# Kernel optimization log

Measured on AMD Instinct MI355X. Metric: run time of the kernel, lower is better.

## Reference

```python
import jax, jax.numpy as jnp
import numpy as np

DIM = 1024
NUM_HEADS = 16
HEAD_DIM = DIM // NUM_HEADS
SCALE = HEAD_DIM ** -0.5
NEG = -1e9


def setup_inputs() -> dict:
    key = jax.random.key(0)
    ks = jax.random.split(key, 10)
    B, N, M, C = 8, 1024, 1024, DIM
    q = jax.random.normal(ks[0], (B, N, C), jnp.float32)
    k = jax.random.normal(ks[1], (B, M, C), jnp.float32)
    v = jax.random.normal(ks[2], (B, M, C), jnp.float32)
    mask = jax.random.randint(ks[3], (B, N), 0, 2, jnp.int32)
    target_mask = jax.random.randint(ks[4], (B, N, M), 0, 2, jnp.int32)
    Wq = jax.random.normal(ks[5], (C, C), jnp.float32) * 0.02
    Wk = jax.random.normal(ks[6], (C, C), jnp.float32) * 0.02
    Wv = jax.random.normal(ks[7], (C, C), jnp.float32) * 0.02
    Wo = jax.random.normal(ks[8], (C, C), jnp.float32) * 0.02
    bo = jnp.zeros((C,), jnp.float32)
    return {"q": q, "k": k, "v": v, "mask": mask, "target_mask": target_mask,
            "Wq": Wq, "Wk": Wk, "Wv": Wv, "Wo": Wo, "bo": bo}


def reference(q, k, v, mask, target_mask, Wq, Wk, Wv, Wo, bo):
    B, N, C = q.shape
    M = k.shape[1]
    H, D = NUM_HEADS, HEAD_DIM
    qh = (q @ Wq).reshape(B, N, H, D)
    kh = (k @ Wk).reshape(B, M, H, D)
    vh = (v @ Wv).reshape(B, M, H, D)
    attn = jnp.einsum('bnhd,bmhd->bhnm', qh, kh) * SCALE  # (B,H,N,M)
    # self-attn key mask (B,N) -> broadcast over queries (requires N==M as in original)
    attn = jnp.where(mask[:, None, None, :] == 0, NEG, attn)
    # cross-attn mask (B,N,M) -> broadcast over heads
    attn = jnp.where(target_mask[:, None, :, :] == 0, NEG, attn)
    attn = jax.nn.softmax(attn, axis=-1)
    x = jnp.einsum('bhnm,bmhd->bnhd', attn, vh).reshape(B, N, C)
    return x @ Wo + bo
```

## Files before the change

### kernel.cpp

```cpp
#include <hip/hip_runtime.h>
#include <hip/hip_bf16.h>

#define DEV __device__ __forceinline__

typedef __attribute__((ext_vector_type(8))) short bf16x8;
typedef __attribute__((ext_vector_type(4))) short s16x4;
typedef __attribute__((ext_vector_type(4))) float f32x4;
typedef unsigned int u32;
typedef unsigned long long u64;

DEV short f2bf(float f) {
  union { float f; u32 u; } x; x.f = f;
  u32 r = x.u + 0x7fffu + ((x.u >> 16) & 1u);
  return (short)(r >> 16);
}

DEV void gload_lds16(const void* g, void* l) {
  __builtin_amdgcn_global_load_lds(
      (const __attribute__((address_space(1))) u32*)g,
      (__attribute__((address_space(3))) u32*)l, 16, 0, 0);
}

__global__ __launch_bounds__(256) void pack_mask(const int* __restrict__ mask,
                                                 const int* __restrict__ tmask,
                                                 u64* __restrict__ pk) {
  int bn = blockIdx.x;
  int b = bn >> 10;
  int t = threadIdx.x, w = t >> 6, lane = t & 63;
  const int* tr = tmask + (size_t)bn * 1024;
  const int* mr = mask + b * 1024;
#pragma unroll
  for (int it = 0; it < 4; ++it) {
    int m = it * 256 + w * 64 + lane;
    bool on = (mr[m] != 0) && (tr[m] != 0);
    u64 bits = __ballot(on);
    if (lane == 0) pk[(size_t)bn * 16 + it * 4 + w] = bits;
  }
}

__global__ __launch_bounds__(256) void wconv_t(const float* __restrict__ W,
                                               short* __restrict__ Wt) {
  __shared__ short tile[64][65];
  int k0 = blockIdx.x * 64, n0 = blockIdx.y * 64;
  int t = threadIdx.x;
  int r = t >> 2, c = (t & 3) * 16;
  const float* src = W + (size_t)(k0 + r) * 1024 + n0 + c;
#pragma unroll
  for (int i = 0; i < 16; i += 4) {
    float4 f = *(const float4*)(src + i);
    tile[r][c + i + 0] = f2bf(f.x);
    tile[r][c + i + 1] = f2bf(f.y);
    tile[r][c + i + 2] = f2bf(f.z);
    tile[r][c + i + 3] = f2bf(f.w);
  }
  __syncthreads();
  bf16x8 v0, v1;
#pragma unroll
  for (int i = 0; i < 8; ++i) v0[i] = tile[c + i][r];
#pragma unroll
  for (int i = 0; i < 8; ++i) v1[i] = tile[c + 8 + i][r];
  short* dst = Wt + (size_t)(n0 + r) * 1024 + k0 + c;
  *(bf16x8*)(dst) = v0;
  *(bf16x8*)(dst + 8) = v1;
}

__global__ __launch_bounds__(256) void vtrans(const short* __restrict__ vh,
                                              short* __restrict__ vht) {
  __shared__ short tile[64][65];
  int m0 = blockIdx.x * 64;
  int bh = blockIdx.y;
  int t = threadIdx.x;
  int r = t >> 2, c = (t & 3) * 16;
  const short* src = vh + ((size_t)bh * 1024 + m0 + r) * 64 + c;
  bf16x8 a0 = *(const bf16x8*)(src);
  bf16x8 a1 = *(const bf16x8*)(src + 8);
#pragma unroll
  for (int i = 0; i < 8; ++i) tile[r][c + i] = a0[i];
#pragma unroll
  for (int i = 0; i < 8; ++i) tile[r][c + 8 + i] = a1[i];
  __syncthreads();
  bf16x8 v0, v1;
#pragma unroll
  for (int i = 0; i < 8; ++i) v0[i] = tile[c + i][r];
#pragma unroll
  for (int i = 0; i < 8; ++i) v1[i] = tile[c + 8 + i][r];
  short* dst = vht + ((size_t)bh * 64 + r) * 1024 + m0 + c;
  *(bf16x8*)dst = v0;
  *(bf16x8*)(dst + 8) = v1;
}

#define QSCALE 0.18033688011112042f

__global__ __launch_bounds__(256, 2) void gemm_qkv(
    const float* __restrict__ Aq, const float* __restrict__ Ak, const float* __restrict__ Av,
    const short* __restrict__ Wqt, const short* __restrict__ Wkt, const short* __restrict__ Wvt,
    short* __restrict__ qh, short* __restrict__ kh, short* __restrict__ vh) {
  int flat = blockIdx.z * 512 + blockIdx.y * 8 + blockIdx.x;
  int nid = (flat & 7) * 192 + (flat >> 3);
  int zz = nid >> 9;
  int rr = nid & 511;
  int bm = (rr >> 3) * 128, bn = (rr & 7) * 128;

  const float* A; const short* Wt; short* Ch; float cs;
  if (zz == 0)      { A = Aq; Wt = Wqt; Ch = qh; cs = QSCALE; }
  else if (zz == 1) { A = Ak; Wt = Wkt; Ch = kh; cs = 1.0f; }
  else              { A = Av; Wt = Wvt; Ch = vh; cs = 1.0f; }

  __shared__ __align__(16) short As[128 * 64];
  __shared__ __align__(16) short Bs[128 * 64];

  int tid = threadIdx.x;
  int lane = tid & 63, w = tid >> 6;
  int wm = w >> 1, wn = w & 1;
  int lr = lane & 15, lg = lane >> 4;

  const f32x4 fz = {0.f, 0.f, 0.f, 0.f};
  f32x4 acc[4][4];
#pragma unroll
  for (int i = 0; i < 4; ++i)
#pragma unroll
    for (int j = 0; j < 4; ++j) acc[i][j] = fz;

  int arow = tid >> 1, ahalf = tid & 1;
  const float* abase = A + (size_t)(bm + arow) * 1024 + ahalf * 32;
  short* adst = &As[arow * 64 + ahalf * 32];
  const char* wbase = (const char*)Wt;

  for (int kt = 0; kt < 1024; kt += 64) {
#pragma unroll
    for (int i = 0; i < 8; ++i) {
      float4 f = *(const float4*)(abase + kt + i * 4);
      s16x4 s;
      s[0] = f2bf(f.x); s[1] = f2bf(f.y); s[2] = f2bf(f.z); s[3] = f2bf(f.w);
      *(s16x4*)(adst + i * 4) = s;
    }
#pragma unroll
    for (int i = 0; i < 4; ++i) {
      int c = w * 4 + i;
      const char* src = wbase + (size_t)(bn + c * 8 + (lane >> 3)) * 2048 + kt * 2 + (lane & 7) * 16;
      gload_lds16(src, (char*)Bs + c * 1024);
    }
    __syncthreads();
#pragma unroll
    for (int ks = 0; ks < 2; ++ks) {
      bf16x8 af[4], bfr[4];
#pragma unroll
      for (int mi = 0; mi < 4; ++mi)
        af[mi] = *(const bf16x8*)&As[(wm * 64 + mi * 16 + lr) * 64 + ks * 32 + lg * 8];
#pragma unroll
      for (int ni = 0; ni < 4; ++ni)
        bfr[ni] = *(const bf16x8*)&Bs[(wn * 64 + ni * 16 + lr) * 64 + ks * 32 + lg * 8];
#pragma unroll
      for (int mi = 0; mi < 4; ++mi)
#pragma unroll
        for (int ni = 0; ni < 4; ++ni)
          acc[mi][ni] = __builtin_amdgcn_mfma_f32_16x16x32_bf16(af[mi], bfr[ni], acc[mi][ni], 0, 0, 0);
    }
    __syncthreads();
  }
#pragma unroll
  for (int mi = 0; mi < 4; ++mi)
#pragma unroll
    for (int ni = 0; ni < 4; ++ni) {
      int ccol = bn + wn * 64 + ni * 16 + lr;
      int h = ccol >> 6, d = ccol & 63;
#pragma unroll
      for (int j = 0; j < 4; ++j) {
        int r = bm + wm * 64 + mi * 16 + lg * 4 + j;
        int bb = r >> 10, n = r & 1023;
        Ch[(((size_t)bb * 16 + h) * 1024 + n) * 64 + d] = f2bf(acc[mi][ni][j] * cs);
      }
    }
}

DEV void stage_kv(const char* kbase, const char* vbase, int kv0,
                  short* Ksb, short* Vsb, int w, int lane) {
#pragma unroll
  for (int i = 0; i < 2; ++i) {
    int c = w * 2 + i;
    int row = (lane >> 3);
    int colb = ((lane & 7) ^ row) << 4;
    gload_lds16(kbase + (size_t)(kv0 + c * 8 + row) * 128 + colb, (char*)Ksb + c * 1024);
    gload_lds16(vbase + (size_t)(c * 8 + row) * 2048 + kv0 * 2 + colb, (char*)Vsb + c * 1024);
  }
}

__global__ __launch_bounds__(256, 2) void attn(
    const short* __restrict__ qh, const short* __restrict__ kh, const short* __restrict__ vht,
    const u64* __restrict__ pk, short* __restrict__ x) {
  __shared__ __align__(16) short Ks[2][4096];
  __shared__ __align__(16) short Vs[2][4096];
  __shared__ __align__(16) short Ps[8192];

  int flat = blockIdx.y * 8 + blockIdx.x;
  int nid = (flat & 7) * 128 + (flat >> 3);
  int bh = nid >> 3, qt = nid & 7;
  int b = bh >> 4;
  int tid = threadIdx.x, lane = tid & 63, w = tid >> 6;
  int lr = lane & 15, lg = lane >> 4;

  bf16x8 qa[2][2];
  {
    const short* qb = qh + ((size_t)bh * 1024 + qt * 128 + w * 32) * 64;
#pragma unroll
    for (int mi = 0; mi < 2; ++mi)
#pragma unroll
      for (int ks = 0; ks < 2; ++ks)
        qa[mi][ks] = *(const bf16x8*)(qb + (mi * 16 + lr) * 64 + ks * 32 + lg * 8);
  }

  const f32x4 fz = {0.f, 0.f, 0.f, 0.f};
  f32x4 o[2][4];
  float psum[2][4];
#pragma unroll
  for (int mi = 0; mi < 2; ++mi)
#pragma unroll
    for (int j = 0; j < 4; ++j) psum[mi][j] = 0.f;
#pragma unroll
  for (int mi = 0; mi < 2; ++mi)
#pragma unroll
    for (int nd = 0; nd < 4; ++nd) o[mi][nd] = fz;

  const char* kbase = (const char*)(kh + (size_t)bh * 65536);
  const char* vbase = (const char*)(vht + (size_t)bh * 65536);
  const u64* pkb = pk + ((size_t)b * 1024 + qt * 128) * 16;

  stage_kv(kbase, vbase, 0, Ks[0], Vs[0], w, lane);
  __syncthreads();
  int cur = 0;

  for (int t = 0; t < 16; ++t) {
    if (t < 15) stage_kv(kbase, vbase, (t + 1) * 64, Ks[cur ^ 1], Vs[cur ^ 1], w, lane);

    u64 pw[2][4];
#pragma unroll
    for (int mi = 0; mi < 2; ++mi)
#pragma unroll
      for (int j = 0; j < 4; ++j)
        pw[mi][j] = pkb[(w * 32 + mi * 16 + lg * 4 + j) * 16 + t];

    f32x4 s[2][4];
#pragma unroll
    for (int mi = 0; mi < 2; ++mi)
#pragma unroll
      for (int ni = 0; ni < 4; ++ni) s[mi][ni] = fz;
#pragma unroll
    for (int ks = 0; ks < 2; ++ks) {
      bf16x8 kb[4];
#pragma unroll
      for (int ni = 0; ni < 4; ++ni)
        kb[ni] = *(const bf16x8*)&Ks[cur][(ni * 16 + lr) * 64 + ((ks * 32 + lg * 8) ^ ((lr & 7) << 3))];
#pragma unroll
      for (int mi = 0; mi < 2; ++mi)
#pragma unroll
        for (int ni = 0; ni < 4; ++ni)
          s[mi][ni] = __builtin_amdgcn_mfma_f32_16x16x32_bf16(qa[mi][ks], kb[ni], s[mi][ni], 0, 0, 0);
    }

#pragma unroll
    for (int mi = 0; mi < 2; ++mi)
#pragma unroll
      for (int j = 0; j < 4; ++j) {
        u32 lo = (u32)pw[mi][j], hi = (u32)(pw[mi][j] >> 32);
        float rs = 0.f;
#pragma unroll
        for (int ni = 0; ni < 4; ++ni) {
          u32 bit = ((ni < 2 ? lo : hi) >> ((ni & 1) * 16 + lr)) & 1u;
          float e = __builtin_amdgcn_exp2f(s[mi][ni][j]);
          float p = bit ? e : 0.f;
          s[mi][ni][j] = p;
          rs += p;
        }
        psum[mi][j] += rs;
      }

#pragma unroll
    for (int mi = 0; mi < 2; ++mi)
#pragma unroll
      for (int j = 0; j < 4; ++j) {
        int r = w * 32 + mi * 16 + lg * 4 + j;
        int sw = (r & 7) << 3;
#pragma unroll
        for (int ni = 0; ni < 4; ++ni)
          Ps[r * 64 + ((ni * 16 + lr) ^ sw)] = f2bf(s[mi][ni][j]);
      }

#pragma unroll
    for (int ks = 0; ks < 2; ++ks) {
      bf16x8 pa[2], vb[4];
#pragma unroll
      for (int mi = 0; mi < 2; ++mi)
        pa[mi] = *(const bf16x8*)&Ps[(w * 32 + mi * 16 + lr) * 64 + ((ks * 32 + lg * 8) ^ ((lr & 7) << 3))];
#pragma unroll
      for (int nd = 0; nd < 4; ++nd)
        vb[nd] = *(const bf16x8*)&Vs[cur][(nd * 16 + lr) * 64 + ((ks * 32 + lg * 8) ^ ((lr & 7) << 3))];
#pragma unroll
      for (int mi = 0; mi < 2; ++mi)
#pragma unroll
        for (int nd = 0; nd < 4; ++nd)
          o[mi][nd] = __builtin_amdgcn_mfma_f32_16x16x32_bf16(pa[mi], vb[nd], o[mi][nd], 0, 0, 0);
    }
    __syncthreads();
    cur ^= 1;
  }

  short* xb = x + ((size_t)b * 1024) * 1024 + (bh & 15) * 64;
#pragma unroll
  for (int mi = 0; mi < 2; ++mi)
#pragma unroll
    for (int j = 0; j < 4; ++j) {
      float rs = psum[mi][j];
#pragma unroll
      for (int dd = 1; dd < 16; dd <<= 1) rs += __shfl_xor(rs, dd, 64);
      float inv = rs > 0.f ? 1.0f / rs : 0.f;
      int qg = qt * 128 + w * 32 + mi * 16 + lg * 4 + j;
#pragma unroll
      for (int nd = 0; nd < 4; ++nd) {
        int d = nd * 16 + lr;
        xb[(size_t)qg * 1024 + d] = f2bf(o[mi][nd][j] * inv);
      }
    }
}

__global__ __launch_bounds__(256, 2) void gemm_out(
    const short* __restrict__ X, const short* __restrict__ Wot,
    const float* __restrict__ bo, float* __restrict__ out) {
  int flat = blockIdx.y * 8 + blockIdx.x;
  int nid = (flat & 7) * 64 + (flat >> 3);
  int bm = (nid >> 3) * 128, bn = (nid & 7) * 128;

  __shared__ __align__(16) short As[128 * 64];
  __shared__ __align__(16) short Bs[128 * 64];
  int tid = threadIdx.x, lane = tid & 63, w = tid >> 6;
  int wm = w >> 1, wn = w & 1, lr = lane & 15, lg = lane >> 4;

  const f32x4 fz = {0.f, 0.f, 0.f, 0.f};
  f32x4 acc[4][4];
#pragma unroll
  for (int i = 0; i < 4; ++i)
#pragma unroll
    for (int j = 0; j < 4; ++j) acc[i][j] = fz;

  const char* xbase = (const char*)X;
  const char* wbase = (const char*)Wot;

  for (int kt = 0; kt < 1024; kt += 64) {
#pragma unroll
    for (int i = 0; i < 4; ++i) {
      int c = w * 4 + i;
      const char* srcA = xbase + (size_t)(bm + c * 8 + (lane >> 3)) * 2048 + kt * 2 + (lane & 7) * 16;
      gload_lds16(srcA, (char*)As + c * 1024);
      const char* srcB = wbase + (size_t)(bn + c * 8 + (lane >> 3)) * 2048 + kt * 2 + (lane & 7) * 16;
      gload_lds16(srcB, (char*)Bs + c * 1024);
    }
    __syncthreads();
#pragma unroll
    for (int ks = 0; ks < 2; ++ks) {
      bf16x8 af[4], bfr[4];
#pragma unroll
      for (int mi = 0; mi < 4; ++mi)
        af[mi] = *(const bf16x8*)&As[(wm * 64 + mi * 16 + lr) * 64 + ks * 32 + lg * 8];
#pragma unroll
      for (int ni = 0; ni < 4; ++ni)
        bfr[ni] = *(const bf16x8*)&Bs[(wn * 64 + ni * 16 + lr) * 64 + ks * 32 + lg * 8];
#pragma unroll
      for (int mi = 0; mi < 4; ++mi)
#pragma unroll
        for (int ni = 0; ni < 4; ++ni)
          acc[mi][ni] = __builtin_amdgcn_mfma_f32_16x16x32_bf16(af[mi], bfr[ni], acc[mi][ni], 0, 0, 0);
    }
    __syncthreads();
  }
#pragma unroll
  for (int mi = 0; mi < 4; ++mi)
#pragma unroll
    for (int ni = 0; ni < 4; ++ni) {
      int ccol = bn + wn * 64 + ni * 16 + lr;
      float bias = bo[ccol];
#pragma unroll
      for (int j = 0; j < 4; ++j) {
        int r = bm + wm * 64 + mi * 16 + lg * 4 + j;
        out[(size_t)r * 1024 + ccol] = acc[mi][ni][j] + bias;
      }
    }
}

extern "C" void kernel_launch(void* const* d_in, const int* in_sizes, int n_in,
                              void* d_out, int out_size, void* d_ws, size_t ws_size,
                              hipStream_t stream) {
  const float* q = (const float*)d_in[0];
  const float* k = (const float*)d_in[1];
  const float* v = (const float*)d_in[2];
  const int* mask = (const int*)d_in[3];
  const int* tmask = (const int*)d_in[4];
  const float* Wq = (const float*)d_in[5];
  const float* Wk = (const float*)d_in[6];
  const float* Wv = (const float*)d_in[7];
  const float* Wo = (const float*)d_in[8];
  const float* bo = (const float*)d_in[9];
  float* out = (float*)d_out;

  char* ws = (char*)d_ws;
  const size_t MB = 1u << 20;
  if (ws_size < 72 * MB) return;
  short* Wqt = (short*)(ws + 0 * MB);
  short* Wkt = (short*)(ws + 2 * MB);
  short* Wvt = (short*)(ws + 4 * MB);
  short* Wot = (short*)(ws + 6 * MB);
  short* qh  = (short*)(ws + 8 * MB);
  short* kh  = (short*)(ws + 24 * MB);
  short* vh  = (short*)(ws + 40 * MB);
  short* vht = (short*)(ws + 56 * MB);
  short* x   = (short*)(ws + 40 * MB);
  u64*   pkb = (u64*)d_out;

  pack_mask<<<dim3(8192), 256, 0, stream>>>(mask, tmask, pkb);
  wconv_t<<<dim3(16, 16), 256, 0, stream>>>(Wq, Wqt);
  wconv_t<<<dim3(16, 16), 256, 0, stream>>>(Wk, Wkt);
  wconv_t<<<dim3(16, 16), 256, 0, stream>>>(Wv, Wvt);
  wconv_t<<<dim3(16, 16), 256, 0, stream>>>(Wo, Wot);

  gemm_qkv<<<dim3(8, 64, 3), 256, 0, stream>>>(q, k, v, Wqt, Wkt, Wvt, qh, kh, vh);
  vtrans<<<dim3(16, 128), 256, 0, stream>>>(vh, vht);
  attn<<<dim3(8, 128), 256, 0, stream>>>(qh, kh, vht, pkb, x);
  gemm_out<<<dim3(8, 64), 256, 0, stream>>>(x, Wot, bo, out);
}
```

Before: 415.1 us.

## Pre-convert activations to bf16 and use swizzled async LDS staging in GEMMs

Adds a separate conversion pass that turns q/k/v fp32 activations into bf16 buffers, so the QKV GEMM can stage A tiles with direct global-to-LDS loads instead of loading fp32 and converting per tile. Both GEMMs now use an XOR-swizzled LDS layout to cut bank conflicts on fragment reads. The four weight conversions are merged into one launch, and buffers are reassigned, with the output buffer reused as scratch for the bf16 activations. This adds an extra read and write pass over the activations in exchange for a lighter GEMM inner loop.

New measurement: 350.7 us. 1.18x faster.

```diff
diff --git a/kernel.cpp b/kernel.cpp
--- a/kernel.cpp
+++ b/kernel.cpp
@@ -4,7 +4,6 @@
 #define DEV __device__ __forceinline__
 
 typedef __attribute__((ext_vector_type(8))) short bf16x8;
-typedef __attribute__((ext_vector_type(4))) short s16x4;
 typedef __attribute__((ext_vector_type(4))) float f32x4;
 typedef unsigned int u32;
 typedef unsigned long long u64;
@@ -19,6 +18,36 @@
   __builtin_amdgcn_global_load_lds(
       (const __attribute__((address_space(1))) u32*)g,
       (__attribute__((address_space(3))) u32*)l, 16, 0, 0);
+}
+
+DEV void stage_t128(const char* base, int ktb, char* lds, int w, int lane) {
+  int r8 = lane >> 3;
+  int csw = ((lane & 7) ^ r8) << 4;
+#pragma unroll
+  for (int i = 0; i < 4; ++i) {
+    int c = w * 4 + i;
+    gload_lds16(base + (size_t)(c * 8 + r8) * 2048 + ktb + csw, lds + c * 1024);
+  }
+}
+
+DEV bf16x8 frag(const short* L, int row, int col) {
+  return *(const bf16x8*)&L[row * 64 + (col ^ ((row & 7) << 3))];
+}
+
+__global__ __launch_bounds__(256) void aconv(const float* __restrict__ q,
+    const float* __restrict__ k, const float* __restrict__ v,
+    short* __restrict__ qb, short* __restrict__ kb, short* __restrict__ vb) {
+  const float* src; short* dst;
+  if (blockIdx.z == 0)      { src = q; dst = qb; }
+  else if (blockIdx.z == 1) { src = k; dst = kb; }
+  else                      { src = v; dst = vb; }
+  size_t i = ((size_t)blockIdx.x * 256 + threadIdx.x) * 8;
+  float4 f0 = *(const float4*)(src + i);
+  float4 f1 = *(const float4*)(src + i + 4);
+  bf16x8 o;
+  o[0] = f2bf(f0.x); o[1] = f2bf(f0.y); o[2] = f2bf(f0.z); o[3] = f2bf(f0.w);
+  o[4] = f2bf(f1.x); o[5] = f2bf(f1.y); o[6] = f2bf(f1.z); o[7] = f2bf(f1.w);
+  *(bf16x8*)(dst + i) = o;
 }
 
 __global__ __launch_bounds__(256) void pack_mask(const int* __restrict__ mask,
@@ -38,8 +67,12 @@
   }
 }
 
-__global__ __launch_bounds__(256) void wconv_t(const float* __restrict__ W,
-                                               short* __restrict__ Wt) {
+__global__ __launch_bounds__(256) void wconv4(const float* __restrict__ W0,
+    const float* __restrict__ W1, const float* __restrict__ W2,
+    const float* __restrict__ W3, short* __restrict__ WtAll) {
+  const float* W = blockIdx.z == 0 ? W0 : blockIdx.z == 1 ? W1
+                 : blockIdx.z == 2 ? W2 : W3;
+  short* Wt = WtAll + (size_t)blockIdx.z * 1024 * 1024;
   __shared__ short tile[64][65];
   int k0 = blockIdx.x * 64, n0 = blockIdx.y * 64;
   int t = threadIdx.x;
@@ -92,8 +125,8 @@
 #define QSCALE 0.18033688011112042f
 
 __global__ __launch_bounds__(256, 2) void gemm_qkv(
-    const float* __restrict__ Aq, const float* __restrict__ Ak, const float* __restrict__ Av,
-    const short* __restrict__ Wqt, const short* __restrict__ Wkt, const short* __restrict__ Wvt,
+    const short* __restrict__ qb, const short* __restrict__ kb, const short* __restrict__ vb,
+    const short* __restrict__ WtAll,
     short* __restrict__ qh, short* __restrict__ kh, short* __restrict__ vh) {
   int flat = blockIdx.z * 512 + blockIdx.y * 8 + blockIdx.x;
   int nid = (flat & 7) * 192 + (flat >> 3);
@@ -101,10 +134,11 @@
   int rr = nid & 511;
   int bm = (rr >> 3) * 128, bn = (rr & 7) * 128;
 
-  const float* A; const short* Wt; short* Ch; float cs;
-  if (zz == 0)      { A = Aq; Wt = Wqt; Ch = qh; cs = QSCALE; }
-  else if (zz == 1) { A = Ak; Wt = Wkt; Ch = kh; cs = 1.0f; }
-  else              { A = Av; Wt = Wvt; Ch = vh; cs = 1.0f; }
+  const short* A; short* Ch; float cs;
+  if (zz == 0)      { A = qb; Ch = qh; cs = QSCALE; }
+  else if (zz == 1) { A = kb; Ch = kh; cs = 1.0f; }
+  else              { A = vb; Ch = vh; cs = 1.0f; }
+  const short* Wt = WtAll + (size_t)zz * 1024 * 1024;
 
   __shared__ __align__(16) short As[128 * 64];
   __shared__ __align__(16) short Bs[128 * 64];
@@ -121,35 +155,22 @@
 #pragma unroll
     for (int j = 0; j < 4; ++j) acc[i][j] = fz;
 
-  int arow = tid >> 1, ahalf = tid & 1;
-  const float* abase = A + (size_t)(bm + arow) * 1024 + ahalf * 32;
-  short* adst = &As[arow * 64 + ahalf * 32];
-  const char* wbase = (const char*)Wt;
-
-  for (int kt = 0; kt < 1024; kt += 64) {
-#pragma unroll
-    for (int i = 0; i < 8; ++i) {
-      float4 f = *(const float4*)(abase + kt + i * 4);
-      s16x4 s;
-      s[0] = f2bf(f.x); s[1] = f2bf(f.y); s[2] = f2bf(f.z); s[3] = f2bf(f.w);
-      *(s16x4*)(adst + i * 4) = s;
-    }
-#pragma unroll
-    for (int i = 0; i < 4; ++i) {
-      int c = w * 4 + i;
-      const char* src = wbase + (size_t)(bn + c * 8 + (lane >> 3)) * 2048 + kt * 2 + (lane & 7) * 16;
-      gload_lds16(src, (char*)Bs + c * 1024);
-    }
+  const char* abase = (const char*)A + (size_t)bm * 2048;
+  const char* bbase = (const char*)Wt + (size_t)bn * 2048;
+
+  for (int ktb = 0; ktb < 2048; ktb += 128) {
+    stage_t128(abase, ktb, (char*)As, w, lane);
+    stage_t128(bbase, ktb, (char*)Bs, w, lane);
     __syncthreads();
 #pragma unroll
     for (int ks = 0; ks < 2; ++ks) {
       bf16x8 af[4], bfr[4];
 #pragma unroll
       for (int mi = 0; mi < 4; ++mi)
-        af[mi] = *(const bf16x8*)&As[(wm * 64 + mi * 16 + lr) * 64 + ks * 32 + lg * 8];
+        af[mi] = frag(As, wm * 64 + mi * 16 + lr, ks * 32 + lg * 8);
 #pragma unroll
       for (int ni = 0; ni < 4; ++ni)
-        bfr[ni] = *(const bf16x8*)&Bs[(wn * 64 + ni * 16 + lr) * 64 + ks * 32 + lg * 8];
+        bfr[ni] = frag(Bs, wn * 64 + ni * 16 + lr, ks * 32 + lg * 8);
 #pragma unroll
       for (int mi = 0; mi < 4; ++mi)
 #pragma unroll
@@ -201,12 +222,12 @@
 
   bf16x8 qa[2][2];
   {
-    const short* qb = qh + ((size_t)bh * 1024 + qt * 128 + w * 32) * 64;
+    const short* qb2 = qh + ((size_t)bh * 1024 + qt * 128 + w * 32) * 64;
 #pragma unroll
     for (int mi = 0; mi < 2; ++mi)
 #pragma unroll
       for (int ks = 0; ks < 2; ++ks)
-        qa[mi][ks] = *(const bf16x8*)(qb + (mi * 16 + lr) * 64 + ks * 32 + lg * 8);
+        qa[mi][ks] = *(const bf16x8*)(qb2 + (mi * 16 + lr) * 64 + ks * 32 + lg * 8);
   }
 
   const f32x4 fz = {0.f, 0.f, 0.f, 0.f};
@@ -246,15 +267,15 @@
       for (int ni = 0; ni < 4; ++ni) s[mi][ni] = fz;
 #pragma unroll
     for (int ks = 0; ks < 2; ++ks) {
-      bf16x8 kb[4];
+      bf16x8 kb2[4];
 #pragma unroll
       for (int ni = 0; ni < 4; ++ni)
-        kb[ni] = *(const bf16x8*)&Ks[cur][(ni * 16 + lr) * 64 + ((ks * 32 + lg * 8) ^ ((lr & 7) << 3))];
+        kb2[ni] = *(const bf16x8*)&Ks[cur][(ni * 16 + lr) * 64 + ((ks * 32 + lg * 8) ^ ((lr & 7) << 3))];
 #pragma unroll
       for (int mi = 0; mi < 2; ++mi)
 #pragma unroll
         for (int ni = 0; ni < 4; ++ni)
-          s[mi][ni] = __builtin_amdgcn_mfma_f32_16x16x32_bf16(qa[mi][ks], kb[ni], s[mi][ni], 0, 0, 0);
+          s[mi][ni] = __builtin_amdgcn_mfma_f32_16x16x32_bf16(qa[mi][ks], kb2[ni], s[mi][ni], 0, 0, 0);
     }
 
 #pragma unroll
@@ -287,18 +308,18 @@
 
 #pragma unroll
     for (int ks = 0; ks < 2; ++ks) {
-      bf16x8 pa[2], vb[4];
+      bf16x8 pa[2], vb2[4];
 #pragma unroll
       for (int mi = 0; mi < 2; ++mi)
         pa[mi] = *(const bf16x8*)&Ps[(w * 32 + mi * 16 + lr) * 64 + ((ks * 32 + lg * 8) ^ ((lr & 7) << 3))];
 #pragma unroll
       for (int nd = 0; nd < 4; ++nd)
-        vb[nd] = *(const bf16x8*)&Vs[cur][(nd * 16 + lr) * 64 + ((ks * 32 + lg * 8) ^ ((lr & 7) << 3))];
+        vb2[nd] = *(const bf16x8*)&Vs[cur][(nd * 16 + lr) * 64 + ((ks * 32 + lg * 8) ^ ((lr & 7) << 3))];
 #pragma unroll
       for (int mi = 0; mi < 2; ++mi)
 #pragma unroll
         for (int nd = 0; nd < 4; ++nd)
-          o[mi][nd] = __builtin_amdgcn_mfma_f32_16x16x32_bf16(pa[mi], vb[nd], o[mi][nd], 0, 0, 0);
+          o[mi][nd] = __builtin_amdgcn_mfma_f32_16x16x32_bf16(pa[mi], vb2[nd], o[mi][nd], 0, 0, 0);
     }
     __syncthreads();
     cur ^= 1;
@@ -341,28 +362,22 @@
 #pragma unroll
     for (int j = 0; j < 4; ++j) acc[i][j] = fz;
 
-  const char* xbase = (const char*)X;
-  const char* wbase = (const char*)Wot;
-
-  for (int kt = 0; kt < 1024; kt += 64) {
-#pragma unroll
-    for (int i = 0; i < 4; ++i) {
-      int c = w * 4 + i;
-      const char* srcA = xbase + (size_t)(bm + c * 8 + (lane >> 3)) * 2048 + kt * 2 + (lane & 7) * 16;
-      gload_lds16(srcA, (char*)As + c * 1024);
-      const char* srcB = wbase + (size_t)(bn + c * 8 + (lane >> 3)) * 2048 + kt * 2 + (lane & 7) * 16;
-      gload_lds16(srcB, (char*)Bs + c * 1024);
-    }
+  const char* abase = (const char*)X + (size_t)bm * 2048;
+  const char* bbase = (const char*)Wot + (size_t)bn * 2048;
+
+  for (int ktb = 0; ktb < 2048; ktb += 128) {
+    stage_t128(abase, ktb, (char*)As, w, lane);
+    stage_t128(bbase, ktb, (char*)Bs, w, lane);
     __syncthreads();
 #pragma unroll
     for (int ks = 0; ks < 2; ++ks) {
       bf16x8 af[4], bfr[4];
 #pragma unroll
       for (int mi = 0; mi < 4; ++mi)
-        af[mi] = *(const bf16x8*)&As[(wm * 64 + mi * 16 + lr) * 64 + ks * 32 + lg * 8];
+        af[mi] = frag(As, wm * 64 + mi * 16 + lr, ks * 32 + lg * 8);
 #pragma unroll
       for (int ni = 0; ni < 4; ++ni)
-        bfr[ni] = *(const bf16x8*)&Bs[(wn * 64 + ni * 16 + lr) * 64 + ks * 32 + lg * 8];
+        bfr[ni] = frag(Bs, wn * 64 + ni * 16 + lr, ks * 32 + lg * 8);
 #pragma unroll
       for (int mi = 0; mi < 4; ++mi)
 #pragma unroll
@@ -402,26 +417,24 @@
 
   char* ws = (char*)d_ws;
   const size_t MB = 1u << 20;
-  if (ws_size < 72 * MB) return;
-  short* Wqt = (short*)(ws + 0 * MB);
-  short* Wkt = (short*)(ws + 2 * MB);
-  short* Wvt = (short*)(ws + 4 * MB);
-  short* Wot = (short*)(ws + 6 * MB);
+  if (ws_size < 73 * MB) return;
+  short* WtAll = (short*)(ws + 0 * MB);
   short* qh  = (short*)(ws + 8 * MB);
   short* kh  = (short*)(ws + 24 * MB);
   short* vh  = (short*)(ws + 40 * MB);
   short* vht = (short*)(ws + 56 * MB);
+  u64*   pkb = (u64*)(ws + 72 * MB);
   short* x   = (short*)(ws + 40 * MB);
-  u64*   pkb = (u64*)d_out;
-
+  short* qbA = (short*)d_out;
+  short* kbA = (short*)d_out + 8 * 1024 * 1024;
+  short* vbA = (short*)(ws + 56 * MB);
+
+  aconv<<<dim3(4096, 1, 3), 256, 0, stream>>>(q, k, v, qbA, kbA, vbA);
+  wconv4<<<dim3(16, 16, 4), 256, 0, stream>>>(Wq, Wk, Wv, Wo, WtAll);
   pack_mask<<<dim3(8192), 256, 0, stream>>>(mask, tmask, pkb);
-  wconv_t<<<dim3(16, 16), 256, 0, stream>>>(Wq, Wqt);
-  wconv_t<<<dim3(16, 16), 256, 0, stream>>>(Wk, Wkt);
-  wconv_t<<<dim3(16, 16), 256, 0, stream>>>(Wv, Wvt);
-  wconv_t<<<dim3(16, 16), 256, 0, stream>>>(Wo, Wot);
-
-  gemm_qkv<<<dim3(8, 64, 3), 256, 0, stream>>>(q, k, v, Wqt, Wkt, Wvt, qh, kh, vh);
+
+  gemm_qkv<<<dim3(8, 64, 3), 256, 0, stream>>>(qbA, kbA, vbA, WtAll, qh, kh, vh);
   vtrans<<<dim3(16, 128), 256, 0, stream>>>(vh, vht);
   attn<<<dim3(8, 128), 256, 0, stream>>>(qh, kh, vht, pkb, x);
-  gemm_out<<<dim3(8, 64), 256, 0, stream>>>(x, Wot, bo, out);
-}
+  gemm_out<<<dim3(8, 64), 256, 0, stream>>>(x, WtAll + 3 * 1024 * 1024, bo, out);
+}
```
